# Optimization experiments

Hardware: AMD Instinct MI355X
Metric: run time of the kernel (lower is better)

Reference implementation:

```python
import jax, jax.numpy as jnp
import numpy as np

N_NODES = 50000
N_EDGES = 800000
D = 64  # node/edge feature dim == out_dim


def _dense_params(key, d_in, d_out):
    kw, kb = jax.random.split(key)
    # flax Dense default: lecun_normal kernel, zero bias
    W = jax.random.normal(kw, (d_in, d_out), dtype=jnp.float32) / np.sqrt(d_in)
    b = jnp.zeros((d_out,), dtype=jnp.float32)
    return W, b


def setup_inputs() -> dict:
    key = jax.random.key(0)
    ks = jax.random.split(key, 10)
    nodes = jax.random.normal(ks[0], (N_NODES, D), dtype=jnp.float32)
    edges = jax.random.normal(ks[1], (N_EDGES, D), dtype=jnp.float32)
    senders = jax.random.randint(ks[2], (N_EDGES,), 0, N_NODES, dtype=jnp.int32)
    receivers = jax.random.randint(ks[3], (N_EDGES,), 0, N_NODES, dtype=jnp.int32)
    W_sent, b_sent = _dense_params(ks[4], D, D)      # sent_attributes_1
    W_recv, b_recv = _dense_params(ks[5], D, D)      # received_attributes
    W_edge, b_edge = _dense_params(ks[6], D, D)      # edge projection
    W_attn, b_attn = _dense_params(ks[7], D, 1)      # attention logit
    W_msg,  b_msg  = _dense_params(ks[8], D, D)      # message Dense (simple_update)
    W_self, b_self = _dense_params(ks[9], D, D)      # self-edge Dense
    return {
        "nodes": nodes, "edges": edges, "senders": senders, "receivers": receivers,
        "W_sent": W_sent, "b_sent": b_sent, "W_recv": W_recv, "b_recv": b_recv,
        "W_edge": W_edge, "b_edge": b_edge, "W_attn": W_attn, "b_attn": b_attn,
        "W_msg": W_msg, "b_msg": b_msg, "W_self": W_self, "b_self": b_self,
    }


def _segment_softmax(logits, segment_ids, num_segments):
    # logits: [E, 1]; stable softmax within each receiver segment
    maxs = jax.ops.segment_max(logits, segment_ids, num_segments=num_segments)
    ex = jnp.exp(logits - maxs[segment_ids])
    sums = jax.ops.segment_sum(ex, segment_ids, num_segments=num_segments)
    return ex / sums[segment_ids]


def reference(nodes, edges, senders, receivers,
              W_sent, b_sent, W_recv, b_recv, W_edge, b_edge,
              W_attn, b_attn, W_msg, b_msg, W_self, b_self):
    # Defaults: simple_update=True -> sync_updates=False, add_features=True,
    # mix_edge_node=False, self_edges=True.
    sent1 = (nodes @ W_sent + b_sent)[senders]          # [E, D]
    sent2 = nodes[senders]                              # [E, D] (simple_update)
    recv  = (nodes @ W_recv + b_recv)[receivers]        # [E, D]
    edge_feat = edges @ W_edge + b_edge                 # [E, D]
    edge_feat = sent1 + edge_feat + recv                # add_features
    logits = jax.nn.leaky_relu(edge_feat @ W_attn + b_attn)   # [E, 1]
    attn = _segment_softmax(logits, receivers, nodes.shape[0])  # [E, 1]
    message = sent2 @ W_msg + b_msg                     # [E, D]
    message = attn * message
    new_nodes = jax.ops.segment_sum(message, receivers, num_segments=nodes.shape[0])
    new_nodes = new_nodes + (nodes @ W_self + b_self)   # self_edges
    return new_nodes, edge_feat
```

## Files before the change

kernel.cpp:

```cpp
#include <hip/hip_runtime.h>
#include <math.h>

constexpr int NN = 50000;
constexpr int NE = 800000;
constexpr int DD = 64;

__device__ __forceinline__ unsigned fmap(float x) {
    unsigned u = __float_as_uint(x);
    return (u & 0x80000000u) ? ~u : (u | 0x80000000u);
}
__device__ __forceinline__ float funmap(unsigned u) {
    unsigned b = (u & 0x80000000u) ? (u & 0x7FFFFFFFu) : ~u;
    return __uint_as_float(b);
}

__device__ __forceinline__ float bcast(float x, int k) {
    return __int_as_float(__builtin_amdgcn_readlane(__float_as_int(x), k));
}

__global__ void k_init(unsigned* __restrict__ segMax, float* __restrict__ segSum) {
    int i = blockIdx.x * blockDim.x + threadIdx.x;
    if (i < NN) { segMax[i] = 0u; segSum[i] = 0.0f; }
}

__global__ __launch_bounds__(256) void k_node(
    const float* __restrict__ nodes,
    const float* __restrict__ Wsent, const float* __restrict__ bsent,
    const float* __restrict__ Wrecv, const float* __restrict__ brecv,
    const float* __restrict__ Wmsg,  const float* __restrict__ bmsg,
    const float* __restrict__ Wself, const float* __restrict__ bself,
    float* __restrict__ sentP, float* __restrict__ recvP,
    float* __restrict__ msgP,  float* __restrict__ selfOut) {
    const int lane = threadIdx.x & 63;
    const int wid  = (blockIdx.x * 256 + threadIdx.x) >> 6;
    const int nw   = (gridDim.x * 256) >> 6;
    const int m    = wid & 3;
    const int w4   = wid >> 2;
    const int nw4  = nw >> 2;

    const float* W; const float* bias; float* out;
    if (m == 0)      { W = Wsent; bias = bsent; out = sentP; }
    else if (m == 1) { W = Wrecv; bias = brecv; out = recvP; }
    else if (m == 2) { W = Wmsg;  bias = bmsg;  out = msgP; }
    else             { W = Wself; bias = bself; out = selfOut; }

    float Wc[DD];
    #pragma unroll
    for (int k = 0; k < DD; ++k) Wc[k] = W[k * DD + lane];
    const float b = bias[lane];

    for (int i = w4; i < NN; i += nw4) {
        float x = nodes[i * DD + lane];
        float a0 = b, a1 = 0.0f;
        #pragma unroll
        for (int k = 0; k < DD; k += 2) {
            a0 += bcast(x, k)     * Wc[k];
            a1 += bcast(x, k + 1) * Wc[k + 1];
        }
        out[i * DD + lane] = a0 + a1;
    }
}

__global__ __launch_bounds__(256) void k_edge(
    const float* __restrict__ edges,
    const int* __restrict__ senders, const int* __restrict__ receivers,
    const float* __restrict__ Wedge, const float* __restrict__ bedge,
    const float* __restrict__ Wattn, const float* __restrict__ battn,
    const float* __restrict__ sentP, const float* __restrict__ recvP,
    float* __restrict__ edgeOut, float* __restrict__ logits,
    unsigned* __restrict__ segMax) {
    const int lane = threadIdx.x & 63;
    const int wid  = (blockIdx.x * 256 + threadIdx.x) >> 6;
    const int nw   = (gridDim.x * 256) >> 6;

    float Wc[DD];
    #pragma unroll
    for (int k = 0; k < DD; ++k) Wc[k] = Wedge[k * DD + lane];
    const float be = bedge[lane];
    const float wa = Wattn[lane];
    const float ba = battn[0];

    for (int e = wid; e < NE; e += nw) {
        float x = edges[(size_t)e * DD + lane];
        int s = senders[e], r = receivers[e];
        float g0 = sentP[s * DD + lane];
        float g1 = recvP[r * DD + lane];
        float a0 = be, a1 = 0.0f, a2 = 0.0f, a3 = 0.0f;
        #pragma unroll
        for (int k = 0; k < DD; k += 4) {
            a0 += bcast(x, k)     * Wc[k];
            a1 += bcast(x, k + 1) * Wc[k + 1];
            a2 += bcast(x, k + 2) * Wc[k + 2];
            a3 += bcast(x, k + 3) * Wc[k + 3];
        }
        float ef = (a0 + a1) + (a2 + a3) + g0 + g1;
        edgeOut[(size_t)e * DD + lane] = ef;
        float t = ef * wa;
        #pragma unroll
        for (int off = 32; off > 0; off >>= 1) t += __shfl_down(t, off, 64);
        if (lane == 0) {
            float v = t + ba;
            v = v > 0.0f ? v : 0.01f * v;
            logits[e] = v;
            atomicMax(segMax + r, fmap(v));
        }
    }
}

__global__ void k_exp(const float* __restrict__ logits,
                      const int* __restrict__ receivers,
                      const unsigned* __restrict__ segMax,
                      float* __restrict__ expv, float* __restrict__ segSum) {
    int e = blockIdx.x * blockDim.x + threadIdx.x;
    if (e < NE) {
        int r = receivers[e];
        float m = funmap(segMax[r]);
        float ex = expf(logits[e] - m);
        expv[e] = ex;
        atomicAdd(segSum + r, ex);
    }
}

__global__ __launch_bounds__(256) void k_scatter(
    const int* __restrict__ senders, const int* __restrict__ receivers,
    const float* __restrict__ expv, const float* __restrict__ segSum,
    const float* __restrict__ msgP, float* __restrict__ outNodes) {
    const int lane = threadIdx.x & 63;
    const int wid  = (blockIdx.x * 256 + threadIdx.x) >> 6;
    const int nw   = (gridDim.x * 256) >> 6;
    for (int e = wid; e < NE; e += nw) {
        int s = senders[e], r = receivers[e];
        float w = expv[e] / segSum[r];
        atomicAdd(outNodes + r * DD + lane, w * msgP[s * DD + lane]);
    }
}

extern "C" void kernel_launch(void* const* d_in, const int* in_sizes, int n_in,
                              void* d_out, int out_size, void* d_ws, size_t ws_size,
                              hipStream_t stream) {
    const float* nodes     = (const float*)d_in[0];
    const float* edges     = (const float*)d_in[1];
    const int*   senders   = (const int*)d_in[2];
    const int*   receivers = (const int*)d_in[3];
    const float* Wsent = (const float*)d_in[4];
    const float* bsent = (const float*)d_in[5];
    const float* Wrecv = (const float*)d_in[6];
    const float* brecv = (const float*)d_in[7];
    const float* Wedge = (const float*)d_in[8];
    const float* bedge = (const float*)d_in[9];
    const float* Wattn = (const float*)d_in[10];
    const float* battn = (const float*)d_in[11];
    const float* Wmsg  = (const float*)d_in[12];
    const float* bmsg  = (const float*)d_in[13];
    const float* Wself = (const float*)d_in[14];
    const float* bself = (const float*)d_in[15];

    float* out = (float*)d_out;
    float* outNodes = out;
    float* outEdge  = out + (size_t)NN * DD;

    float* ws = (float*)d_ws;
    float* sentP  = ws;
    float* recvP  = sentP + (size_t)NN * DD;
    float* msgP   = recvP + (size_t)NN * DD;
    float* logits = msgP  + (size_t)NN * DD;
    float* expv   = logits + NE;
    float* segSum = expv + NE;
    unsigned* segMax = (unsigned*)(segSum + NN);

    k_init<<<(NN + 255) / 256, 256, 0, stream>>>(segMax, segSum);
    k_node<<<512, 256, 0, stream>>>(nodes, Wsent, bsent, Wrecv, brecv,
                                    Wmsg, bmsg, Wself, bself,
                                    sentP, recvP, msgP, outNodes);
    k_edge<<<4096, 256, 0, stream>>>(edges, senders, receivers, Wedge, bedge,
                                     Wattn, battn, sentP, recvP,
                                     outEdge, logits, segMax);
    k_exp<<<(NE + 255) / 256, 256, 0, stream>>>(logits, receivers, segMax, expv, segSum);
    k_scatter<<<4096, 256, 0, stream>>>(senders, receivers, expv, segSum, msgP, outNodes);
}
```

Measured before the change: 869.9 us.

## Replace atomic segment softmax/scatter with CSR gather and thread-per-row matmuls

Builds a receiver-sorted CSR index (count, single-block scan, atomic fill) and computes segment max, sum and the weighted message aggregation per node in one wave, with no float atomics. The node and edge projections switch from a wave-per-row readlane broadcast to a thread-per-row layout with a 64-float register accumulator and float4 loads and stores, and the separate exp kernel is removed. This trades atomic contention on the output for extra index-building kernels, a serial single-block scan, strided per-thread row reads, and heavy register pressure in the matmul kernels.

```diff
diff --git a/kernel.cpp b/kernel.cpp
--- a/kernel.cpp
+++ b/kernel.cpp
@@ -5,22 +5,56 @@
 constexpr int NE = 800000;
 constexpr int DD = 64;
 
-__device__ __forceinline__ unsigned fmap(float x) {
-    unsigned u = __float_as_uint(x);
-    return (u & 0x80000000u) ? ~u : (u | 0x80000000u);
-}
-__device__ __forceinline__ float funmap(unsigned u) {
-    unsigned b = (u & 0x80000000u) ? (u & 0x7FFFFFFFu) : ~u;
-    return __uint_as_float(b);
-}
-
-__device__ __forceinline__ float bcast(float x, int k) {
-    return __int_as_float(__builtin_amdgcn_readlane(__float_as_int(x), k));
-}
-
-__global__ void k_init(unsigned* __restrict__ segMax, float* __restrict__ segSum) {
+__device__ __forceinline__ float wave_max(float v) {
+    #pragma unroll
+    for (int off = 32; off > 0; off >>= 1) v = fmaxf(v, __shfl_xor(v, off, 64));
+    return v;
+}
+__device__ __forceinline__ float wave_sum(float v) {
+    #pragma unroll
+    for (int off = 32; off > 0; off >>= 1) v += __shfl_xor(v, off, 64);
+    return v;
+}
+
+__global__ void k_init(int* __restrict__ deg) {
     int i = blockIdx.x * blockDim.x + threadIdx.x;
-    if (i < NN) { segMax[i] = 0u; segSum[i] = 0.0f; }
+    if (i < NN) deg[i] = 0;
+}
+
+__global__ void k_count(const int* __restrict__ receivers, int* __restrict__ deg) {
+    int e = blockIdx.x * blockDim.x + threadIdx.x;
+    if (e < NE) atomicAdd(deg + receivers[e], 1);
+}
+
+__global__ __launch_bounds__(1024) void k_scan(const int* __restrict__ deg,
+                                               int* __restrict__ starts) {
+    __shared__ int buf0[1024], buf1[1024];
+    const int t = threadIdx.x;
+    constexpr int C = (NN + 1023) / 1024;
+    int lo = t * C; if (lo > NN) lo = NN;
+    int hi = lo + C; if (hi > NN) hi = NN;
+    int s = 0;
+    for (int i = lo; i < hi; ++i) s += deg[i];
+    buf0[t] = s;
+    __syncthreads();
+    int* src = buf0; int* dst = buf1;
+    for (int off = 1; off < 1024; off <<= 1) {
+        int v = src[t] + ((t >= off) ? src[t - off] : 0);
+        dst[t] = v;
+        __syncthreads();
+        int* tmp = src; src = dst; dst = tmp;
+    }
+    int run = (t == 0) ? 0 : src[t - 1];
+    for (int i = lo; i < hi; ++i) { starts[i] = run; run += deg[i]; }
+}
+
+__global__ void k_fill(const int* __restrict__ receivers,
+                       int* __restrict__ starts, int* __restrict__ eidx) {
+    int e = blockIdx.x * blockDim.x + threadIdx.x;
+    if (e < NE) {
+        int pos = atomicAdd(starts + receivers[e], 1);
+        eidx[pos] = e;
+    }
 }
 
 __global__ __launch_bounds__(256) void k_node(
@@ -32,11 +66,10 @@
     float* __restrict__ sentP, float* __restrict__ recvP,
     float* __restrict__ msgP,  float* __restrict__ selfOut) {
     const int lane = threadIdx.x & 63;
-    const int wid  = (blockIdx.x * 256 + threadIdx.x) >> 6;
-    const int nw   = (gridDim.x * 256) >> 6;
-    const int m    = wid & 3;
-    const int w4   = wid >> 2;
-    const int nw4  = nw >> 2;
+    const int w = (blockIdx.x * 256 + threadIdx.x) >> 6;
+    const int m = w / 782;
+    const int i = (w % 782) * 64 + lane;
+    if (i >= NN) return;
 
     const float* W; const float* bias; float* out;
     if (m == 0)      { W = Wsent; bias = bsent; out = sentP; }
@@ -44,20 +77,31 @@
     else if (m == 2) { W = Wmsg;  bias = bmsg;  out = msgP; }
     else             { W = Wself; bias = bself; out = selfOut; }
 
-    float Wc[DD];
-    #pragma unroll
-    for (int k = 0; k < DD; ++k) Wc[k] = W[k * DD + lane];
-    const float b = bias[lane];
-
-    for (int i = w4; i < NN; i += nw4) {
-        float x = nodes[i * DD + lane];
-        float a0 = b, a1 = 0.0f;
+    float acc[DD];
+    #pragma unroll
+    for (int j = 0; j < DD; ++j) acc[j] = bias[j];
+
+    const float* xrow = nodes + (size_t)i * DD;
+    for (int kc = 0; kc < 4; ++kc) {
+        float4 x0 = *(const float4*)(xrow + kc * 16 + 0);
+        float4 x1 = *(const float4*)(xrow + kc * 16 + 4);
+        float4 x2 = *(const float4*)(xrow + kc * 16 + 8);
+        float4 x3 = *(const float4*)(xrow + kc * 16 + 12);
+        float xs[16] = {x0.x, x0.y, x0.z, x0.w, x1.x, x1.y, x1.z, x1.w,
+                        x2.x, x2.y, x2.z, x2.w, x3.x, x3.y, x3.z, x3.w};
         #pragma unroll
-        for (int k = 0; k < DD; k += 2) {
-            a0 += bcast(x, k)     * Wc[k];
-            a1 += bcast(x, k + 1) * Wc[k + 1];
+        for (int kk = 0; kk < 16; ++kk) {
+            const float* Wr = W + (kc * 16 + kk) * DD;
+            #pragma unroll
+            for (int j = 0; j < DD; ++j) acc[j] += xs[kk] * Wr[j];
         }
-        out[i * DD + lane] = a0 + a1;
+    }
+    float* orow = out + (size_t)i * DD;
+    #pragma unroll
+    for (int j4 = 0; j4 < DD / 4; ++j4) {
+        float4 v; v.x = acc[j4*4+0]; v.y = acc[j4*4+1];
+                  v.z = acc[j4*4+2]; v.w = acc[j4*4+3];
+        *(float4*)(orow + j4 * 4) = v;
     }
 }
 
@@ -67,72 +111,84 @@
     const float* __restrict__ Wedge, const float* __restrict__ bedge,
     const float* __restrict__ Wattn, const float* __restrict__ battn,
     const float* __restrict__ sentP, const float* __restrict__ recvP,
-    float* __restrict__ edgeOut, float* __restrict__ logits,
-    unsigned* __restrict__ segMax) {
+    float* __restrict__ edgeOut, float* __restrict__ logits) {
     const int lane = threadIdx.x & 63;
-    const int wid  = (blockIdx.x * 256 + threadIdx.x) >> 6;
-    const int nw   = (gridDim.x * 256) >> 6;
-
-    float Wc[DD];
-    #pragma unroll
-    for (int k = 0; k < DD; ++k) Wc[k] = Wedge[k * DD + lane];
-    const float be = bedge[lane];
-    const float wa = Wattn[lane];
-    const float ba = battn[0];
-
-    for (int e = wid; e < NE; e += nw) {
-        float x = edges[(size_t)e * DD + lane];
-        int s = senders[e], r = receivers[e];
-        float g0 = sentP[s * DD + lane];
-        float g1 = recvP[r * DD + lane];
-        float a0 = be, a1 = 0.0f, a2 = 0.0f, a3 = 0.0f;
+    const int w = (blockIdx.x * 256 + threadIdx.x) >> 6;
+    const int e = w * 64 + lane;
+
+    float acc[DD];
+    #pragma unroll
+    for (int j = 0; j < DD; ++j) acc[j] = bedge[j];
+
+    const float* xrow = edges + (size_t)e * DD;
+    for (int kc = 0; kc < 4; ++kc) {
+        float4 x0 = *(const float4*)(xrow + kc * 16 + 0);
+        float4 x1 = *(const float4*)(xrow + kc * 16 + 4);
+        float4 x2 = *(const float4*)(xrow + kc * 16 + 8);
+        float4 x3 = *(const float4*)(xrow + kc * 16 + 12);
+        float xs[16] = {x0.x, x0.y, x0.z, x0.w, x1.x, x1.y, x1.z, x1.w,
+                        x2.x, x2.y, x2.z, x2.w, x3.x, x3.y, x3.z, x3.w};
         #pragma unroll
-        for (int k = 0; k < DD; k += 4) {
-            a0 += bcast(x, k)     * Wc[k];
-            a1 += bcast(x, k + 1) * Wc[k + 1];
-            a2 += bcast(x, k + 2) * Wc[k + 2];
-            a3 += bcast(x, k + 3) * Wc[k + 3];
+        for (int kk = 0; kk < 16; ++kk) {
+            const float* Wr = Wedge + (kc * 16 + kk) * DD;
+            #pragma unroll
+            for (int j = 0; j < DD; ++j) acc[j] += xs[kk] * Wr[j];
         }
-        float ef = (a0 + a1) + (a2 + a3) + g0 + g1;
-        edgeOut[(size_t)e * DD + lane] = ef;
-        float t = ef * wa;
-        #pragma unroll
-        for (int off = 32; off > 0; off >>= 1) t += __shfl_down(t, off, 64);
-        if (lane == 0) {
-            float v = t + ba;
-            v = v > 0.0f ? v : 0.01f * v;
-            logits[e] = v;
-            atomicMax(segMax + r, fmap(v));
-        }
-    }
-}
-
-__global__ void k_exp(const float* __restrict__ logits,
-                      const int* __restrict__ receivers,
-                      const unsigned* __restrict__ segMax,
-                      float* __restrict__ expv, float* __restrict__ segSum) {
-    int e = blockIdx.x * blockDim.x + threadIdx.x;
-    if (e < NE) {
-        int r = receivers[e];
-        float m = funmap(segMax[r]);
-        float ex = expf(logits[e] - m);
-        expv[e] = ex;
-        atomicAdd(segSum + r, ex);
-    }
-}
-
-__global__ __launch_bounds__(256) void k_scatter(
-    const int* __restrict__ senders, const int* __restrict__ receivers,
-    const float* __restrict__ expv, const float* __restrict__ segSum,
+    }
+
+    const int s = senders[e];
+    const int r = receivers[e];
+    const float* srow = sentP + (size_t)s * DD;
+    const float* rrow = recvP + (size_t)r * DD;
+    float* orow = edgeOut + (size_t)e * DD;
+    float t = 0.0f;
+    #pragma unroll
+    for (int j4 = 0; j4 < DD / 4; ++j4) {
+        float4 sv = *(const float4*)(srow + j4 * 4);
+        float4 rv = *(const float4*)(rrow + j4 * 4);
+        float4 ev;
+        ev.x = acc[j4*4+0] + sv.x + rv.x;
+        ev.y = acc[j4*4+1] + sv.y + rv.y;
+        ev.z = acc[j4*4+2] + sv.z + rv.z;
+        ev.w = acc[j4*4+3] + sv.w + rv.w;
+        t += ev.x * Wattn[j4*4+0] + ev.y * Wattn[j4*4+1]
+           + ev.z * Wattn[j4*4+2] + ev.w * Wattn[j4*4+3];
+        *(float4*)(orow + j4 * 4) = ev;
+    }
+    float v = t + battn[0];
+    v = v > 0.0f ? v : 0.01f * v;
+    logits[e] = v;
+}
+
+__global__ __launch_bounds__(256) void k_final(
+    const int* __restrict__ startsAfter, const int* __restrict__ eidx,
+    const int* __restrict__ senders, const float* __restrict__ logits,
     const float* __restrict__ msgP, float* __restrict__ outNodes) {
     const int lane = threadIdx.x & 63;
-    const int wid  = (blockIdx.x * 256 + threadIdx.x) >> 6;
-    const int nw   = (gridDim.x * 256) >> 6;
-    for (int e = wid; e < NE; e += nw) {
-        int s = senders[e], r = receivers[e];
-        float w = expv[e] / segSum[r];
-        atomicAdd(outNodes + r * DD + lane, w * msgP[s * DD + lane]);
-    }
+    const int n = (blockIdx.x * 256 + threadIdx.x) >> 6;
+    if (n >= NN) return;
+    const int end = startsAfter[n];
+    const int beg = (n > 0) ? startsAfter[n - 1] : 0;
+
+    float mloc = -1e30f;
+    for (int b = beg + lane; b < end; b += 64)
+        mloc = fmaxf(mloc, logits[eidx[b]]);
+    const float m = wave_max(mloc);
+
+    float sloc = 0.0f;
+    for (int b = beg + lane; b < end; b += 64)
+        sloc += expf(logits[eidx[b]] - m);
+    const float denom = wave_sum(sloc);
+    const float inv = 1.0f / denom;
+
+    float acc = 0.0f;
+    for (int b = beg; b < end; ++b) {
+        const int e = eidx[b];
+        const float wgt = expf(logits[e] - m) * inv;
+        const int s = senders[e];
+        acc += wgt * msgP[(size_t)s * DD + lane];
+    }
+    outNodes[(size_t)n * DD + lane] += acc;
 }
 
 extern "C" void kernel_launch(void* const* d_in, const int* in_sizes, int n_in,
@@ -164,17 +220,20 @@
     float* recvP  = sentP + (size_t)NN * DD;
     float* msgP   = recvP + (size_t)NN * DD;
     float* logits = msgP  + (size_t)NN * DD;
-    float* expv   = logits + NE;
-    float* segSum = expv + NE;
-    unsigned* segMax = (unsigned*)(segSum + NN);
-
-    k_init<<<(NN + 255) / 256, 256, 0, stream>>>(segMax, segSum);
-    k_node<<<512, 256, 0, stream>>>(nodes, Wsent, bsent, Wrecv, brecv,
-                                    Wmsg, bmsg, Wself, bself,
-                                    sentP, recvP, msgP, outNodes);
-    k_edge<<<4096, 256, 0, stream>>>(edges, senders, receivers, Wedge, bedge,
-                                     Wattn, battn, sentP, recvP,
-                                     outEdge, logits, segMax);
-    k_exp<<<(NE + 255) / 256, 256, 0, stream>>>(logits, receivers, segMax, expv, segSum);
-    k_scatter<<<4096, 256, 0, stream>>>(senders, receivers, expv, segSum, msgP, outNodes);
-}
+    int*   deg    = (int*)(logits + NE);
+    int*   starts = deg + NN;
+    int*   eidx   = starts + NN;
+
+    k_init <<<(NN + 255) / 256, 256, 0, stream>>>(deg);
+    k_count<<<(NE + 255) / 256, 256, 0, stream>>>(receivers, deg);
+    k_scan <<<1, 1024, 0, stream>>>(deg, starts);
+    k_fill <<<(NE + 255) / 256, 256, 0, stream>>>(receivers, starts, eidx);
+    k_node <<<782, 256, 0, stream>>>(nodes, Wsent, bsent, Wrecv, brecv,
+                                     Wmsg, bmsg, Wself, bself,
+                                     sentP, recvP, msgP, outNodes);
+    k_edge <<<3125, 256, 0, stream>>>(edges, senders, receivers, Wedge, bedge,
+                                      Wattn, battn, sentP, recvP,
+                                      outEdge, logits);
+    k_final<<<(NN * 64 + 255) / 256, 256, 0, stream>>>(starts, eidx, senders,
+                                                       logits, msgP, outNodes);
+}
```

New measurement: 1.045 ms. 1.2x slower.
